# Kernel tuning notes

Measured on AMD Instinct MI355X. Metric: run time of the kernel, lower is better.

## Reference

```python
import jax, jax.numpy as jnp
import numpy as np

B, CIN, F, H, W = 4, 256, 128, 64, 64
EPS = 1e-5

def _conv1x1(x, Wm, b):
    # x: [B,C,H,W], Wm: [O,C] (1x1 conv kernel), b: [O]
    return jnp.einsum('bchw,oc->bohw', x, Wm) + b[None, :, None, None]

def setup_inputs() -> dict:
    key = jax.random.key(0)
    ks = jax.random.split(key, 11)
    s_in = 1.0 / np.sqrt(CIN)
    s_f = 1.0 / np.sqrt(F)
    return {
        'x':    jax.random.normal(ks[0], (B, CIN, H, W), jnp.float32),
        'Wg':   jax.random.normal(ks[1], (F, CIN), jnp.float32) * s_in,
        'bg':   jax.random.normal(ks[2], (F,), jnp.float32) * s_in,
        'Wt':   jax.random.normal(ks[3], (F, CIN), jnp.float32) * s_in,
        'bt':   jax.random.normal(ks[4], (F,), jnp.float32) * s_in,
        'Wp':   jax.random.normal(ks[5], (F, CIN), jnp.float32) * s_in,
        'bp':   jax.random.normal(ks[6], (F,), jnp.float32) * s_in,
        'Wz':   jax.random.normal(ks[7], (CIN, F), jnp.float32) * s_f,
        'bz':   jax.random.normal(ks[8], (CIN,), jnp.float32) * s_f,
        'ln_w': jax.random.normal(ks[9], (CIN, H, W), jnp.float32) * 0.1,
        'ln_b': jax.random.normal(ks[10], (CIN, H, W), jnp.float32) * 0.1,
    }

def reference(x, Wg, bg, Wt, bt, Wp, bp, Wz, bz, ln_w, ln_b):
    b, _, h, w = x.shape
    n = h * w
    # 1x1 conv projections
    g = _conv1x1(x, Wg, bg).reshape(b, F, n).transpose(0, 2, 1)      # [B,N,F]
    theta = _conv1x1(x, Wt, bt).reshape(b, F, n).transpose(0, 2, 1)  # [B,N,F]
    phi = _conv1x1(x, Wp, bp).reshape(b, F, n)                        # [B,F,N]
    # embedded-Gaussian affinity + softmax attention
    f = jnp.einsum('bnf,bfm->bnm', theta, phi)                        # [B,N,N]
    attn = jax.nn.softmax(f, axis=-1)
    y = jnp.einsum('bnm,bmf->bnf', attn, g)                           # [B,N,F]
    y = y.transpose(0, 2, 1).reshape(b, F, h, w)                      # [B,F,H,W]
    # output projection
    z = _conv1x1(y, Wz, bz)                                           # [B,CIN,H,W]
    # LayerNorm over (C,H,W) per sample, affine params shaped [C,H,W]
    mu = jnp.mean(z, axis=(1, 2, 3), keepdims=True)
    var = jnp.var(z, axis=(1, 2, 3), keepdims=True)
    z = (z - mu) * jax.lax.rsqrt(var + EPS)
    z = z * ln_w[None] + ln_b[None]
    return z + x
```

## Files before the change

kernel.cpp:

```cpp
#include <hip/hip_runtime.h>
#include <stdint.h>

#define CIN 256
#define FDIM 128
#define NSP 4096
#define EPS 1e-5f

typedef __attribute__((ext_vector_type(8))) short short8;
typedef __attribute__((ext_vector_type(4))) float f32x4;
typedef __attribute__((ext_vector_type(16))) float f32x16;

__device__ __forceinline__ short f2bf(float f) {
  union { float f; uint32_t u; } v; v.f = f;
  uint32_t r = v.u + 0x7fffu + ((v.u >> 16) & 1u);
  return (short)(r >> 16);
}
__device__ __forceinline__ float bf2f(short h) {
  union { uint32_t u; float f; } v; v.u = ((uint32_t)(uint16_t)h) << 16;
  return v.f;
}

__global__ void prep_all(const float* __restrict__ x,
                         const float* __restrict__ Wg, const float* __restrict__ Wt,
                         const float* __restrict__ Wp, const float* __restrict__ Wz,
                         short* __restrict__ xT, short* __restrict__ Wbf,
                         short* __restrict__ Wzbf, float* __restrict__ sums) {
  __shared__ float tile[32][33];
  int bx = blockIdx.x;
  if (bx < 4096) {
    int b = bx >> 10, c0 = ((bx >> 7) & 7) * 32, n0 = (bx & 127) * 32;
    int r = threadIdx.x >> 5, c = threadIdx.x & 31;
    const float* xb = x + (size_t)b * CIN * NSP;
#pragma unroll
    for (int k = 0; k < 4; k++)
      tile[r + 8 * k][c] = xb[(size_t)(c0 + r + 8 * k) * NSP + n0 + c];
    __syncthreads();
    short* xTb = xT + (size_t)b * NSP * CIN;
#pragma unroll
    for (int k = 0; k < 4; k++)
      xTb[(size_t)(n0 + r + 8 * k) * CIN + c0 + c] = f2bf(tile[c][r + 8 * k]);
  } else {
    int wb = bx - 4096;
    if (wb == 0 && threadIdx.x < 8) sums[threadIdx.x] = 0.f;
    int u = wb * 256 + threadIdx.x;
    if (u < 12288) {
      int p = u >> 12;
      int rem = u & 4095;
      int ftg = rem >> 9, s = (rem >> 6) & 7, lane = rem & 63;
      int row = ftg * 16 + (lane & 15);
      int col = s * 32 + (lane >> 4) * 8;
      const float* Wsrc = (p == 0) ? Wt : (p == 1) ? Wp : Wg;
      short8 v8;
#pragma unroll
      for (int j = 0; j < 8; j++) v8[j] = f2bf(Wsrc[row * 256 + col + j]);
      *(short8*)(Wbf + (size_t)u * 8) = v8;
    } else if (u < 12288 + 4096) {
      int u2 = u - 12288;
      int cog = u2 >> 8, s = (u2 >> 6) & 3, lane = u2 & 63;
      int co = cog * 16 + (lane & 15);
      int ch = s * 32 + (lane >> 4) * 8;
      short8 v8;
#pragma unroll
      for (int j = 0; j < 8; j++) v8[j] = f2bf(Wz[co * 128 + ch + j]);
      *(short8*)(Wzbf + (size_t)u2 * 8) = v8;
    }
  }
}

__global__ void __launch_bounds__(256)
proj_kernel(const short* __restrict__ xT, const short* __restrict__ Wbf,
            const float* __restrict__ bt, const float* __restrict__ bp,
            const float* __restrict__ bg,
            short* __restrict__ theta, short* __restrict__ Kb, short* __restrict__ gT) {
  __shared__ short Axy[32 * 264];
  __shared__ short lds[5120];
  int bx = blockIdx.x;
  int b = bx >> 7;
  int n0 = (bx & 127) << 5;
  int p = blockIdx.y;
  int t = threadIdx.x, w = t >> 6, lane = t & 63, l15 = lane & 15, quad = lane >> 4;

  const short* src = xT + (size_t)(b * NSP + n0) * CIN;
#pragma unroll
  for (int sweep = 0; sweep < 4; sweep++) {
    int i = sweep * 256 + t;
    int row = i >> 5, c16 = i & 31;
    *(short8*)(Axy + row * 264 + c16 * 8) = *(const short8*)(src + i * 8);
  }
  __syncthreads();

  short8 a[8];
  int ar = (w & 1) * 16 + l15;
#pragma unroll
  for (int s = 0; s < 8; s++)
    a[s] = *(const short8*)(Axy + ar * 264 + s * 32 + quad * 8);

  const short* Wsrc = Wbf + p * 32768;
  f32x4 zero = {0.f, 0.f, 0.f, 0.f};
  f32x4 acc[4];
#pragma unroll
  for (int i = 0; i < 4; i++) acc[i] = zero;

#pragma unroll
  for (int s = 0; s < 8; s++) {
#pragma unroll
    for (int ft = 0; ft < 4; ft++) {
      int ftg = (w >> 1) * 4 + ft;
      short8 bfr = *(const short8*)(Wsrc + (ftg * 8 + s) * 512 + lane * 8);
      acc[ft] = __builtin_amdgcn_mfma_f32_16x16x32_bf16(a[s], bfr, acc[ft], 0, 0, 0);
    }
  }

  const float* bias = (p == 0) ? bt : (p == 1) ? bp : bg;
  if (p < 2) {
#pragma unroll
    for (int ft = 0; ft < 4; ft++) {
      int ftg = (w >> 1) * 4 + ft;
      float bv = bias[ftg * 16 + l15];
#pragma unroll
      for (int rr = 0; rr < 4; rr++) {
        int n = (w & 1) * 16 + quad * 4 + rr;
        lds[n * 136 + ftg * 16 + l15] = f2bf(acc[ft][rr] + bv);
      }
    }
    __syncthreads();
    short* dst = ((p == 0) ? theta : Kb) + (size_t)(b * NSP + n0) * FDIM;
#pragma unroll
    for (int i = 0; i < 2; i++) {
      int flat = t + 256 * i;
      int row = flat >> 4, ch = flat & 15;
      *(short8*)(dst + (size_t)row * FDIM + ch * 8) = *(const short8*)(lds + row * 136 + ch * 8);
    }
  } else {
#pragma unroll
    for (int ft = 0; ft < 4; ft++) {
      int ftg = (w >> 1) * 4 + ft;
      float bv = bias[ftg * 16 + l15];
#pragma unroll
      for (int rr = 0; rr < 4; rr++) {
        int n = (w & 1) * 16 + quad * 4 + rr;
        lds[(ftg * 16 + l15) * 40 + n] = f2bf(acc[ft][rr] + bv);
      }
    }
    __syncthreads();
    short* dst = gT + (size_t)b * FDIM * NSP + n0;
#pragma unroll
    for (int i = 0; i < 2; i++) {
      int flat = t + 256 * i;
      int f = flat >> 2, c = flat & 3;
      *(short8*)(dst + (size_t)f * NSP + c * 8) = *(const short8*)(lds + f * 40 + c * 8);
    }
  }
}

__global__ void __launch_bounds__(256, 2)
flash_kernel(const short* __restrict__ thetab, const short* __restrict__ Kb,
             const short* __restrict__ gT, short* __restrict__ opart,
             float* __restrict__ lpart) {
  __shared__ __attribute__((aligned(16))) char smem[34816];
  short* Klds = (short*)smem;
  short* Vlds = (short*)(smem + 16384);

  const int bx = blockIdx.x;
  const int b  = bx >> 7;
  const int r  = bx & 127;
  const int q0 = (r >> 2) << 7;
  const int kc = r & 3;
  const int t = threadIdx.x, w = t >> 6, lane = t & 63;
  const int l31 = lane & 31, h = lane >> 5;
  const int qw = q0 + w * 32;

  const short* Qsrc = thetab + (size_t)b * NSP * FDIM;
  const short* Ksrc = Kb + (size_t)b * NSP * FDIM;
  const short* Vsrc = gT + (size_t)b * FDIM * NSP;

  short8 qf[8];
#pragma unroll
  for (int s = 0; s < 8; s++)
    qf[s] = *(const short8*)(Qsrc + (size_t)(qw + l31) * FDIM + s * 16 + h * 8);

  f32x16 O[4];
#pragma unroll
  for (int i = 0; i < 4; i++)
#pragma unroll
    for (int j = 0; j < 16; j++) O[i][j] = 0.f;
  float lsum = 0.f;

  const int kr0 = t >> 4, kcc0 = t & 15, kr1 = kr0 + 16;
  const int woK0 = kcc0 * 256 + ((kr0 ^ (kcc0 & 7)) * 8);
  const int woK1 = kcc0 * 256 + ((kr1 ^ (kcc0 & 7)) * 8);
  const int vf0 = t >> 2, vcc0 = t & 3, vf1 = 64 + (t >> 2);
  const int woV0 = vcc0 * 1024 + ((vf0 ^ (vcc0 & 3)) * 8);
  const int woV1 = vcc0 * 1024 + ((vf1 ^ (vcc0 & 3)) * 8);

  const int kA0 = kc << 10;
  short8 rKa0, rKa1, rKb0, rKb1, rVa0, rVa1, rVb0, rVb1;

  {
    rKa0 = *(const short8*)(Ksrc + (size_t)(kA0 + kr0) * FDIM + kcc0 * 8);
    rKa1 = *(const short8*)(Ksrc + (size_t)(kA0 + kr1) * FDIM + kcc0 * 8);
    rKb0 = *(const short8*)(Ksrc + (size_t)(kA0 + 32 + kr0) * FDIM + kcc0 * 8);
    rKb1 = *(const short8*)(Ksrc + (size_t)(kA0 + 32 + kr1) * FDIM + kcc0 * 8);
    rVa0 = *(const short8*)(Vsrc + (size_t)vf0 * NSP + kA0 + vcc0 * 8);
    rVa1 = *(const short8*)(Vsrc + (size_t)vf1 * NSP + kA0 + vcc0 * 8);
    rVb0 = *(const short8*)(Vsrc + (size_t)vf0 * NSP + kA0 + 32 + vcc0 * 8);
    rVb1 = *(const short8*)(Vsrc + (size_t)vf1 * NSP + kA0 + 32 + vcc0 * 8);
    *(short8*)(Klds + woK0) = rKa0;
    *(short8*)(Klds + woK1) = rKa1;
    *(short8*)(Klds + 4096 + woK0) = rKb0;
    *(short8*)(Klds + 4096 + woK1) = rKb1;
    *(short8*)(Vlds + woV0) = rVa0;
    *(short8*)(Vlds + woV1) = rVa1;
    *(short8*)(Vlds + 4096 + woV0) = rVb0;
    *(short8*)(Vlds + 4096 + woV1) = rVb1;
  }

#pragma unroll 2
  for (int it = 0; it < 16; ++it) {
    __syncthreads();
    if (it < 15) {
      int kn = kA0 + (it + 1) * 64;
      rKa0 = *(const short8*)(Ksrc + (size_t)(kn + kr0) * FDIM + kcc0 * 8);
      rKa1 = *(const short8*)(Ksrc + (size_t)(kn + kr1) * FDIM + kcc0 * 8);
      rKb0 = *(const short8*)(Ksrc + (size_t)(kn + 32 + kr0) * FDIM + kcc0 * 8);
      rKb1 = *(const short8*)(Ksrc + (size_t)(kn + 32 + kr1) * FDIM + kcc0 * 8);
      rVa0 = *(const short8*)(Vsrc + (size_t)vf0 * NSP + kn + vcc0 * 8);
      rVa1 = *(const short8*)(Vsrc + (size_t)vf1 * NSP + kn + vcc0 * 8);
      rVb0 = *(const short8*)(Vsrc + (size_t)vf0 * NSP + kn + 32 + vcc0 * 8);
      rVb1 = *(const short8*)(Vsrc + (size_t)vf1 * NSP + kn + 32 + vcc0 * 8);
    }

    f32x16 S0, S1;
#pragma unroll
    for (int j = 0; j < 16; j++) { S0[j] = 0.f; S1[j] = 0.f; }
    __builtin_amdgcn_s_setprio(1);
#pragma unroll
    for (int s = 0; s < 8; s++) {
      int c = 2 * s + h;
      const short* base = Klds + c * 256 + ((l31 ^ (c & 7)) * 8);
      short8 ak0 = *(const short8*)(base);
      short8 ak1 = *(const short8*)(base + 4096);
      S0 = __builtin_amdgcn_mfma_f32_32x32x16_bf16(ak0, qf[s], S0, 0, 0, 0);
      S1 = __builtin_amdgcn_mfma_f32_32x32x16_bf16(ak1, qf[s], S1, 0, 0, 0);
    }
    __builtin_amdgcn_s_setprio(0);

    short8 AfA[2], AfB[2];
#pragma unroll
    for (int sub = 0; sub < 2; sub++) {
      float p[16];
#pragma unroll
      for (int i = 0; i < 16; i++) p[i] = __expf(sub ? S1[i] : S0[i]);
      float t8[8];
#pragma unroll
      for (int i = 0; i < 8; i++) t8[i] = p[2 * i] + p[2 * i + 1];
      lsum += ((t8[0] + t8[1]) + (t8[2] + t8[3])) + ((t8[4] + t8[5]) + (t8[6] + t8[7]));

      uint32_t W[8];
#pragma unroll
      for (int j = 0; j < 8; j++)
        asm("v_cvt_pk_bf16_f32 %0, %1, %2" : "=v"(W[j]) : "v"(p[2 * j]), "v"(p[2 * j + 1]));
      asm("v_permlane32_swap_b32 %0, %1" : "+v"(W[0]), "+v"(W[2]));
      asm("v_permlane32_swap_b32 %0, %1" : "+v"(W[1]), "+v"(W[3]));
      asm("v_permlane32_swap_b32 %0, %1" : "+v"(W[4]), "+v"(W[6]));
      asm("v_permlane32_swap_b32 %0, %1" : "+v"(W[5]), "+v"(W[7]));
      union { short8 s; uint32_t u[4]; } u0, u1;
      u0.u[0] = W[0]; u0.u[1] = W[1]; u0.u[2] = W[2]; u0.u[3] = W[3];
      u1.u[0] = W[4]; u1.u[1] = W[5]; u1.u[2] = W[6]; u1.u[3] = W[7];
      if (sub) { AfB[0] = u0.s; AfB[1] = u1.s; }
      else     { AfA[0] = u0.s; AfA[1] = u1.s; }
    }

    __builtin_amdgcn_s_setprio(1);
#pragma unroll
    for (int ft = 0; ft < 4; ft++) {
#pragma unroll
      for (int tt = 0; tt < 2; tt++) {
        int c = tt * 2 + h;
        int off = c * 1024 + ft * 256 + ((l31 ^ (c & 3)) * 8);
        short8 bva = *(const short8*)(Vlds + off);
        O[ft] = __builtin_amdgcn_mfma_f32_32x32x16_bf16(AfA[tt], bva, O[ft], 0, 0, 0);
        short8 bvb = *(const short8*)(Vlds + off + 4096);
        O[ft] = __builtin_amdgcn_mfma_f32_32x32x16_bf16(AfB[tt], bvb, O[ft], 0, 0, 0);
      }
    }
    __builtin_amdgcn_s_setprio(0);

    __syncthreads();
    if (it < 15) {
      *(short8*)(Klds + woK0) = rKa0;
      *(short8*)(Klds + woK1) = rKa1;
      *(short8*)(Klds + 4096 + woK0) = rKb0;
      *(short8*)(Klds + 4096 + woK1) = rKb1;
      *(short8*)(Vlds + woV0) = rVa0;
      *(short8*)(Vlds + woV1) = rVa1;
      *(short8*)(Vlds + 4096 + woV0) = rVb0;
      *(short8*)(Vlds + 4096 + woV1) = rVb1;
    }
  }

  lsum += __shfl_xor(lsum, 32, 64);

  short* tr = (short*)smem + w * 32 * 136;
#pragma unroll
  for (int ft = 0; ft < 4; ft++) {
#pragma unroll
    for (int reg = 0; reg < 16; reg++) {
      int rowq = (reg & 3) + 8 * (reg >> 2) + 4 * h;
      tr[rowq * 136 + ft * 32 + l31] = f2bf(O[ft][reg]);
    }
  }
  short* od = opart + ((size_t)(kc * 4 + b) * NSP + qw) * FDIM;
#pragma unroll
  for (int i = 0; i < 8; i++) {
    int slot = lane + 64 * i;
    int row = slot >> 4, c = slot & 15;
    *(short8*)(od + (size_t)row * FDIM + c * 8) = *(const short8*)(tr + row * 136 + c * 8);
  }
  if (h == 0) lpart[(size_t)(kc * 4 + b) * NSP + qw + l31] = lsum;
}

__global__ void __launch_bounds__(256)
zproj_kernel(const short* __restrict__ opart, const float* __restrict__ lpart,
             const short* __restrict__ Wzbf, const float* __restrict__ bz,
             short* __restrict__ zb, float* __restrict__ sums) {
  __shared__ short Alds[32 * 136];
  __shared__ short ldsT[128 * 40];
  __shared__ float Linv[32];
  __shared__ float wsum[4][2];
  int bx = blockIdx.x;
  int b = bx >> 7;
  int n0 = (bx & 127) << 5;
  int ch0 = blockIdx.y * 128;
  int t = threadIdx.x, w = t >> 6, lane = t & 63, l15 = lane & 15, quad = lane >> 4;

  if (t < 32) {
    float L = 0.f;
#pragma unroll
    for (int kcc = 0; kcc < 4; kcc++) L += lpart[(size_t)(kcc * 4 + b) * NSP + n0 + t];
    Linv[t] = 1.0f / L;
  }
  __syncthreads();

#pragma unroll
  for (int iter = 0; iter < 2; iter++) {
    int i = t + 256 * iter;
    int row = i >> 4, c16 = i & 15;
    const short* base = opart + ((size_t)b * NSP + n0 + row) * FDIM + c16 * 8;
    float accv[8] = {0, 0, 0, 0, 0, 0, 0, 0};
#pragma unroll
    for (int kcc = 0; kcc < 4; kcc++) {
      short8 v = *(const short8*)(base + (size_t)kcc * 4 * NSP * FDIM);
#pragma unroll
      for (int j = 0; j < 8; j++) accv[j] += bf2f(v[j]);
    }
    float inv = Linv[row];
    short8 av;
#pragma unroll
    for (int j = 0; j < 8; j++) av[j] = f2bf(accv[j] * inv);
    *(short8*)(Alds + row * 136 + c16 * 8) = av;
  }
  __syncthreads();

  short8 a[4];
#pragma unroll
  for (int s = 0; s < 4; s++)
    a[s] = *(const short8*)(Alds + ((w & 1) * 16 + l15) * 136 + s * 32 + quad * 8);

  f32x4 zero = {0.f, 0.f, 0.f, 0.f};
  f32x4 acc[4];
#pragma unroll
  for (int i = 0; i < 4; i++) acc[i] = zero;
#pragma unroll
  for (int s = 0; s < 4; s++) {
#pragma unroll
    for (int ct = 0; ct < 4; ct++) {
      int cog = blockIdx.y * 8 + (w >> 1) * 4 + ct;
      short8 bfr = *(const short8*)(Wzbf + cog * 2048 + s * 512 + lane * 8);
      acc[ct] = __builtin_amdgcn_mfma_f32_16x16x32_bf16(a[s], bfr, acc[ct], 0, 0, 0);
    }
  }

  float s1 = 0.0f, s2 = 0.0f;
#pragma unroll
  for (int ct = 0; ct < 4; ct++) {
    int cg = (w >> 1) * 64 + ct * 16 + l15;
    float bv = bz[ch0 + cg];
#pragma unroll
    for (int rr = 0; rr < 4; rr++) {
      float v = acc[ct][rr] + bv;
      s1 += v; s2 += v * v;
      ldsT[cg * 40 + (w & 1) * 16 + quad * 4 + rr] = f2bf(v);
    }
  }
#pragma unroll
  for (int off = 32; off >= 1; off >>= 1) {
    s1 += __shfl_xor(s1, off, 64);
    s2 += __shfl_xor(s2, off, 64);
  }
  if (lane == 0) { wsum[w][0] = s1; wsum[w][1] = s2; }
  __syncthreads();
  if (t == 0) {
    atomicAdd(&sums[b * 2],     wsum[0][0] + wsum[1][0] + wsum[2][0] + wsum[3][0]);
    atomicAdd(&sums[b * 2 + 1], wsum[0][1] + wsum[1][1] + wsum[2][1] + wsum[3][1]);
  }
  short* dst = zb + (size_t)b * CIN * NSP + (size_t)ch0 * NSP + n0;
#pragma unroll
  for (int i = 0; i < 2; i++) {
    int flat = t + 256 * i;
    int c = flat >> 2, ch = flat & 3;
    *(short8*)(dst + (size_t)c * NSP + ch * 8) = *(const short8*)(ldsT + c * 40 + ch * 8);
  }
}

__global__ void __launch_bounds__(256)
finalize_kernel(const short* __restrict__ zbuf, const float* __restrict__ x,
                const float* __restrict__ lnw, const float* __restrict__ lnb,
                const float* __restrict__ sums, float* __restrict__ out) {
  int gid = blockIdx.x * 256 + threadIdx.x;
  size_t e0 = (size_t)gid * 8;
  int b = (int)(e0 >> 20);
  size_t ib = e0 & ((size_t)(1u << 20) - 1);
  float mean = sums[b * 2] * (1.0f / 1048576.0f);
  float var = sums[b * 2 + 1] * (1.0f / 1048576.0f) - mean * mean;
  float rs = rsqrtf(var + EPS);
  short8 zv = *(const short8*)(zbuf + e0);
  f32x4 xv0 = *(const f32x4*)(x + e0),   xv1 = *(const f32x4*)(x + e0 + 4);
  f32x4 wv0 = *(const f32x4*)(lnw + ib), wv1 = *(const f32x4*)(lnw + ib + 4);
  f32x4 bv0 = *(const f32x4*)(lnb + ib), bv1 = *(const f32x4*)(lnb + ib + 4);
  f32x4 o0, o1;
#pragma unroll
  for (int k = 0; k < 4; k++) {
    o0[k] = (bf2f(zv[k]) - mean) * rs * wv0[k] + bv0[k] + xv0[k];
    o1[k] = (bf2f(zv[k + 4]) - mean) * rs * wv1[k] + bv1[k] + xv1[k];
  }
  *(f32x4*)(out + e0) = o0;
  *(f32x4*)(out + e0 + 4) = o1;
}

extern "C" void kernel_launch(void* const* d_in, const int* in_sizes, int n_in,
                              void* d_out, int out_size, void* d_ws, size_t ws_size,
                              hipStream_t stream) {
  const float* x   = (const float*)d_in[0];
  const float* Wg  = (const float*)d_in[1];
  const float* bg  = (const float*)d_in[2];
  const float* Wt  = (const float*)d_in[3];
  const float* bt  = (const float*)d_in[4];
  const float* Wp  = (const float*)d_in[5];
  const float* bp  = (const float*)d_in[6];
  const float* Wz  = (const float*)d_in[7];
  const float* bz  = (const float*)d_in[8];
  const float* lnw = (const float*)d_in[9];
  const float* lnb = (const float*)d_in[10];
  float* out = (float*)d_out;

  char* ws = (char*)d_ws;
  short* Wbf    = (short*)(ws);
  short* Wzbf   = (short*)(ws + 196608);
  short* xT     = (short*)(ws + 262144);
  short* opart  = (short*)(ws + 262144);
  float* lpart  = (float*)(ws + 17039360);
  short* thetab = (short*)(ws + 17301504);
  short* Kb     = (short*)(ws + 21495808);
  short* gT     = (short*)(ws + 25690112);
  short* zb     = (short*)(ws + 17301504);
  float* sums   = (float*)(ws + 29884416);

  prep_all<<<4160, 256, 0, stream>>>(x, Wg, Wt, Wp, Wz, xT, Wbf, Wzbf, sums);
  proj_kernel<<<dim3(512, 3), 256, 0, stream>>>(xT, Wbf, bt, bp, bg, thetab, Kb, gT);
  flash_kernel<<<512, 256, 0, stream>>>(thetab, Kb, gT, opart, lpart);
  zproj_kernel<<<dim3(512, 2), 256, 0, stream>>>(opart, lpart, Wzbf, bz, zb, sums);
  finalize_kernel<<<2048, 256, 0, stream>>>(zb, x, lnw, lnb, sums, out);
}
```

Baseline: 182.7 us.

## Fuse x transpose/bf16 cast into projection kernel and merge three projections per block

The x transpose and bf16 conversion move out of the prep kernel and into proj_kernel, which now reads fp32 x directly through an LDS tile. The xT intermediate buffer and its global write/read round-trip go away. Each block also computes all three projections (theta, phi, g) in a loop, reusing the A fragments in registers instead of launching three grid rows that each reload x. The trade-off is fewer blocks (512 instead of 1536), more serial work and barriers per block, and strided fp32 loads of x.

```diff
diff --git a/kernel.cpp b/kernel.cpp
--- a/kernel.cpp
+++ b/kernel.cpp
@@ -20,74 +20,62 @@
   return v.f;
 }
 
-__global__ void prep_all(const float* __restrict__ x,
-                         const float* __restrict__ Wg, const float* __restrict__ Wt,
-                         const float* __restrict__ Wp, const float* __restrict__ Wz,
-                         short* __restrict__ xT, short* __restrict__ Wbf,
-                         short* __restrict__ Wzbf, float* __restrict__ sums) {
-  __shared__ float tile[32][33];
-  int bx = blockIdx.x;
-  if (bx < 4096) {
-    int b = bx >> 10, c0 = ((bx >> 7) & 7) * 32, n0 = (bx & 127) * 32;
-    int r = threadIdx.x >> 5, c = threadIdx.x & 31;
-    const float* xb = x + (size_t)b * CIN * NSP;
-#pragma unroll
-    for (int k = 0; k < 4; k++)
-      tile[r + 8 * k][c] = xb[(size_t)(c0 + r + 8 * k) * NSP + n0 + c];
-    __syncthreads();
-    short* xTb = xT + (size_t)b * NSP * CIN;
-#pragma unroll
-    for (int k = 0; k < 4; k++)
-      xTb[(size_t)(n0 + r + 8 * k) * CIN + c0 + c] = f2bf(tile[c][r + 8 * k]);
-  } else {
-    int wb = bx - 4096;
-    if (wb == 0 && threadIdx.x < 8) sums[threadIdx.x] = 0.f;
-    int u = wb * 256 + threadIdx.x;
-    if (u < 12288) {
-      int p = u >> 12;
-      int rem = u & 4095;
-      int ftg = rem >> 9, s = (rem >> 6) & 7, lane = rem & 63;
-      int row = ftg * 16 + (lane & 15);
-      int col = s * 32 + (lane >> 4) * 8;
-      const float* Wsrc = (p == 0) ? Wt : (p == 1) ? Wp : Wg;
-      short8 v8;
-#pragma unroll
-      for (int j = 0; j < 8; j++) v8[j] = f2bf(Wsrc[row * 256 + col + j]);
-      *(short8*)(Wbf + (size_t)u * 8) = v8;
-    } else if (u < 12288 + 4096) {
-      int u2 = u - 12288;
-      int cog = u2 >> 8, s = (u2 >> 6) & 3, lane = u2 & 63;
-      int co = cog * 16 + (lane & 15);
-      int ch = s * 32 + (lane >> 4) * 8;
-      short8 v8;
-#pragma unroll
-      for (int j = 0; j < 8; j++) v8[j] = f2bf(Wz[co * 128 + ch + j]);
-      *(short8*)(Wzbf + (size_t)u2 * 8) = v8;
-    }
+__global__ void prep_w(const float* __restrict__ Wg, const float* __restrict__ Wt,
+                       const float* __restrict__ Wp, const float* __restrict__ Wz,
+                       short* __restrict__ Wbf, short* __restrict__ Wzbf,
+                       float* __restrict__ sums) {
+  int u = blockIdx.x * 256 + threadIdx.x;
+  if (u < 8 && blockIdx.x == 0) sums[u] = 0.f;
+  if (u < 12288) {
+    int p = u >> 12;
+    int rem = u & 4095;
+    int ftg = rem >> 9, s = (rem >> 6) & 7, lane = rem & 63;
+    int row = ftg * 16 + (lane & 15);
+    int col = s * 32 + (lane >> 4) * 8;
+    const float* Wsrc = (p == 0) ? Wt : (p == 1) ? Wp : Wg;
+    short8 v8;
+#pragma unroll
+    for (int j = 0; j < 8; j++) v8[j] = f2bf(Wsrc[row * 256 + col + j]);
+    *(short8*)(Wbf + (size_t)u * 8) = v8;
+  } else if (u < 12288 + 4096) {
+    int u2 = u - 12288;
+    int cog = u2 >> 8, s = (u2 >> 6) & 3, lane = u2 & 63;
+    int co = cog * 16 + (lane & 15);
+    int ch = s * 32 + (lane >> 4) * 8;
+    short8 v8;
+#pragma unroll
+    for (int j = 0; j < 8; j++) v8[j] = f2bf(Wz[co * 128 + ch + j]);
+    *(short8*)(Wzbf + (size_t)u2 * 8) = v8;
   }
 }
 
 __global__ void __launch_bounds__(256)
-proj_kernel(const short* __restrict__ xT, const short* __restrict__ Wbf,
+proj_kernel(const float* __restrict__ x, const short* __restrict__ Wbf,
             const float* __restrict__ bt, const float* __restrict__ bp,
             const float* __restrict__ bg,
             short* __restrict__ theta, short* __restrict__ Kb, short* __restrict__ gT) {
+  __shared__ float tile[32][33];
   __shared__ short Axy[32 * 264];
   __shared__ short lds[5120];
   int bx = blockIdx.x;
   int b = bx >> 7;
   int n0 = (bx & 127) << 5;
-  int p = blockIdx.y;
   int t = threadIdx.x, w = t >> 6, lane = t & 63, l15 = lane & 15, quad = lane >> 4;
-
-  const short* src = xT + (size_t)(b * NSP + n0) * CIN;
-#pragma unroll
-  for (int sweep = 0; sweep < 4; sweep++) {
-    int i = sweep * 256 + t;
-    int row = i >> 5, c16 = i & 31;
-    *(short8*)(Axy + row * 264 + c16 * 8) = *(const short8*)(src + i * 8);
-  }
-  __syncthreads();
+  int r = t >> 5, cc = t & 31;
+
+  const float* xb = x + (size_t)b * CIN * NSP;
+#pragma unroll
+  for (int ch = 0; ch < 8; ch++) {
+    int c0 = ch * 32;
+#pragma unroll
+    for (int k = 0; k < 4; k++)
+      tile[r + 8 * k][cc] = xb[(size_t)(c0 + r + 8 * k) * NSP + n0 + cc];
+    __syncthreads();
+#pragma unroll
+    for (int k = 0; k < 4; k++)
+      Axy[(r + 8 * k) * 264 + c0 + cc] = f2bf(tile[cc][r + 8 * k]);
+    __syncthreads();
+  }
 
   short8 a[8];
   int ar = (w & 1) * 16 + l15;
@@ -95,60 +83,63 @@
   for (int s = 0; s < 8; s++)
     a[s] = *(const short8*)(Axy + ar * 264 + s * 32 + quad * 8);
 
-  const short* Wsrc = Wbf + p * 32768;
-  f32x4 zero = {0.f, 0.f, 0.f, 0.f};
-  f32x4 acc[4];
-#pragma unroll
-  for (int i = 0; i < 4; i++) acc[i] = zero;
-
-#pragma unroll
-  for (int s = 0; s < 8; s++) {
-#pragma unroll
-    for (int ft = 0; ft < 4; ft++) {
-      int ftg = (w >> 1) * 4 + ft;
-      short8 bfr = *(const short8*)(Wsrc + (ftg * 8 + s) * 512 + lane * 8);
-      acc[ft] = __builtin_amdgcn_mfma_f32_16x16x32_bf16(a[s], bfr, acc[ft], 0, 0, 0);
-    }
-  }
-
-  const float* bias = (p == 0) ? bt : (p == 1) ? bp : bg;
-  if (p < 2) {
-#pragma unroll
-    for (int ft = 0; ft < 4; ft++) {
-      int ftg = (w >> 1) * 4 + ft;
-      float bv = bias[ftg * 16 + l15];
-#pragma unroll
-      for (int rr = 0; rr < 4; rr++) {
-        int n = (w & 1) * 16 + quad * 4 + rr;
-        lds[n * 136 + ftg * 16 + l15] = f2bf(acc[ft][rr] + bv);
-      }
-    }
-    __syncthreads();
-    short* dst = ((p == 0) ? theta : Kb) + (size_t)(b * NSP + n0) * FDIM;
-#pragma unroll
-    for (int i = 0; i < 2; i++) {
-      int flat = t + 256 * i;
-      int row = flat >> 4, ch = flat & 15;
-      *(short8*)(dst + (size_t)row * FDIM + ch * 8) = *(const short8*)(lds + row * 136 + ch * 8);
-    }
-  } else {
-#pragma unroll
-    for (int ft = 0; ft < 4; ft++) {
-      int ftg = (w >> 1) * 4 + ft;
-      float bv = bias[ftg * 16 + l15];
-#pragma unroll
-      for (int rr = 0; rr < 4; rr++) {
-        int n = (w & 1) * 16 + quad * 4 + rr;
-        lds[(ftg * 16 + l15) * 40 + n] = f2bf(acc[ft][rr] + bv);
-      }
-    }
-    __syncthreads();
-    short* dst = gT + (size_t)b * FDIM * NSP + n0;
-#pragma unroll
-    for (int i = 0; i < 2; i++) {
-      int flat = t + 256 * i;
-      int f = flat >> 2, c = flat & 3;
-      *(short8*)(dst + (size_t)f * NSP + c * 8) = *(const short8*)(lds + f * 40 + c * 8);
+  for (int p = 0; p < 3; p++) {
+    const short* Wsrc = Wbf + p * 32768;
+    f32x4 zero = {0.f, 0.f, 0.f, 0.f};
+    f32x4 acc[4];
+#pragma unroll
+    for (int i = 0; i < 4; i++) acc[i] = zero;
+
+#pragma unroll
+    for (int s = 0; s < 8; s++) {
+#pragma unroll
+      for (int ft = 0; ft < 4; ft++) {
+        int ftg = (w >> 1) * 4 + ft;
+        short8 bfr = *(const short8*)(Wsrc + (ftg * 8 + s) * 512 + lane * 8);
+        acc[ft] = __builtin_amdgcn_mfma_f32_16x16x32_bf16(a[s], bfr, acc[ft], 0, 0, 0);
+      }
+    }
+
+    const float* bias = (p == 0) ? bt : (p == 1) ? bp : bg;
+    if (p > 0) __syncthreads();
+    if (p < 2) {
+#pragma unroll
+      for (int ft = 0; ft < 4; ft++) {
+        int ftg = (w >> 1) * 4 + ft;
+        float bv = bias[ftg * 16 + l15];
+#pragma unroll
+        for (int rr = 0; rr < 4; rr++) {
+          int n = (w & 1) * 16 + quad * 4 + rr;
+          lds[n * 136 + ftg * 16 + l15] = f2bf(acc[ft][rr] + bv);
+        }
+      }
+      __syncthreads();
+      short* dst = ((p == 0) ? theta : Kb) + (size_t)(b * NSP + n0) * FDIM;
+#pragma unroll
+      for (int i = 0; i < 2; i++) {
+        int flat = t + 256 * i;
+        int row = flat >> 4, ch = flat & 15;
+        *(short8*)(dst + (size_t)row * FDIM + ch * 8) = *(const short8*)(lds + row * 136 + ch * 8);
+      }
+    } else {
+#pragma unroll
+      for (int ft = 0; ft < 4; ft++) {
+        int ftg = (w >> 1) * 4 + ft;
+        float bv = bias[ftg * 16 + l15];
+#pragma unroll
+        for (int rr = 0; rr < 4; rr++) {
+          int n = (w & 1) * 16 + quad * 4 + rr;
+          lds[(ftg * 16 + l15) * 40 + n] = f2bf(acc[ft][rr] + bv);
+        }
+      }
+      __syncthreads();
+      short* dst = gT + (size_t)b * FDIM * NSP + n0;
+#pragma unroll
+      for (int i = 0; i < 2; i++) {
+        int flat = t + 256 * i;
+        int f = flat >> 2, c = flat & 3;
+        *(short8*)(dst + (size_t)f * NSP + c * 8) = *(const short8*)(lds + f * 40 + c * 8);
+      }
     }
   }
 }
@@ -457,7 +448,6 @@
   char* ws = (char*)d_ws;
   short* Wbf    = (short*)(ws);
   short* Wzbf   = (short*)(ws + 196608);
-  short* xT     = (short*)(ws + 262144);
   short* opart  = (short*)(ws + 262144);
   float* lpart  = (float*)(ws + 17039360);
   short* thetab = (short*)(ws + 17301504);
@@ -466,8 +456,8 @@
   short* zb     = (short*)(ws + 17301504);
   float* sums   = (float*)(ws + 29884416);
 
-  prep_all<<<4160, 256, 0, stream>>>(x, Wg, Wt, Wp, Wz, xT, Wbf, Wzbf, sums);
-  proj_kernel<<<dim3(512, 3), 256, 0, stream>>>(xT, Wbf, bt, bp, bg, thetab, Kb, gT);
+  prep_w<<<64, 256, 0, stream>>>(Wg, Wt, Wp, Wz, Wbf, Wzbf, sums);
+  proj_kernel<<<512, 256, 0, stream>>>(x, Wbf, bt, bp, bg, thetab, Kb, gT);
   flash_kernel<<<512, 256, 0, stream>>>(thetab, Kb, gT, opart, lpart);
   zproj_kernel<<<dim3(512, 2), 256, 0, stream>>>(opart, lpart, Wzbf, bz, zb, sums);
   finalize_kernel<<<2048, 256, 0, stream>>>(zb, x, lnw, lnb, sums, out);
```

After: 180.5 us (median of 2 runs). Within noise of the previous version (-1.2%).
